# Kernel tuning notes

Hardware: AMD Instinct MI355X
Metric: run time of the kernel (lower is better)

The kernel has to match this reference:

```python
import math
import jax, jax.numpy as jnp
import numpy as np

B, T, C = 2, 2048, 2048
H, G = 16, 4          # n_head, n_group
HKV = H // G          # kv heads
HD = C // H           # head dim = 128

def setup_inputs() -> dict:
    key = jax.random.key(0)
    ks = jax.random.split(key, 4)
    s = 0.02  # realistic init scale
    return {
        "x": jax.random.normal(ks[0], (B, T, C), jnp.float32),
        "Wkv": jax.random.normal(ks[1], (C, 2 * C // G), jnp.float32) * s,
        "bkv": jnp.zeros((2 * C // G,), jnp.float32),
        "Wq": jax.random.normal(ks[2], (C, C), jnp.float32) * s,
        "bq": jnp.zeros((C,), jnp.float32),
        "Wp": jax.random.normal(ks[3], (C, C), jnp.float32) * s,
        "bp": jnp.zeros((C,), jnp.float32),
    }

def _expand_kv(t):
    # (B,T,HKV*HD) -> replicate each kv head G times -> (B,H,T,HD)
    t = t.reshape(B, T, HKV, HD)
    t = jnp.broadcast_to(t[:, :, None], (B, T, G, HKV, HD)).reshape(B, T, H, HD)
    return t.transpose(0, 2, 1, 3)

def reference(x, Wkv, bkv, Wq, bq, Wp, bp):
    kv = x @ Wkv + bkv                      # (B,T,2C/G)
    k, v = jnp.split(kv, 2, axis=-1)
    q = (x @ Wq + bq).reshape(B, T, H, HD).transpose(0, 2, 1, 3)  # (B,H,T,HD)
    k = _expand_kv(k)
    v = _expand_kv(v)
    att = jnp.einsum('bhqd,bhkd->bhqk', q, k) * (1.0 / math.sqrt(HD))
    mask = jnp.tril(jnp.ones((T, T), bool))
    att = jnp.where(mask, att, -jnp.inf)
    att = jax.nn.softmax(att, axis=-1)
    y = jnp.einsum('bhqk,bhkd->bhqd', att, v)
    y = y.transpose(0, 2, 1, 3).reshape(B, T, C)
    return y @ Wp + bp
```

## Files before the change

### kernel.cpp

```cpp
#include <hip/hip_runtime.h>

#define Bv 2
#define Tv 2048
#define Cv 2048
#define Hv 16
#define HKVv 4
#define HDv 128

typedef __attribute__((ext_vector_type(8))) __bf16 bf16x8;
typedef __attribute__((ext_vector_type(4))) float floatx4;

__device__ __forceinline__ unsigned short f2b(float f) {
  unsigned int x = __float_as_uint(f);
  x += 0x7fffu + ((x >> 16) & 1u);
  return (unsigned short)(x >> 16);
}

#define MFMA(a, b, c) __builtin_amdgcn_mfma_f32_16x16x32_bf16((a), (b), (c), 0, 0, 0)

__device__ __forceinline__ void gld_lds16(const void* g, void* l) {
  __builtin_amdgcn_global_load_lds((const __attribute__((address_space(1))) void*)g,
                                   (__attribute__((address_space(3))) void*)l, 16, 0, 0);
}

__global__ void cvt_kernel(const float* __restrict__ src, unsigned short* __restrict__ dst, int n4) {
  int i = blockIdx.x * blockDim.x + threadIdx.x;
  if (i < n4) {
    float4 f = ((const float4*)src)[i];
    ushort4 u;
    u.x = f2b(f.x); u.y = f2b(f.y); u.z = f2b(f.z); u.w = f2b(f.w);
    ((ushort4*)dst)[i] = u;
  }
}

__global__ void tcvt_kernel(const float* __restrict__ src, unsigned short* __restrict__ dst, int K, int N) {
  __shared__ float tile[32][33];
  int k0 = blockIdx.x * 32, n0 = blockIdx.y * 32;
  int tx = threadIdx.x, ty = threadIdx.y;
  for (int i = ty; i < 32; i += 8)
    tile[i][tx] = src[(size_t)(k0 + i) * N + n0 + tx];
  __syncthreads();
  for (int i = ty; i < 32; i += 8)
    dst[(size_t)(n0 + i) * K + k0 + tx] = f2b(tile[tx][i]);
}

__global__ __launch_bounds__(256) void gemm_qkv(
    const unsigned short* __restrict__ xb,
    const unsigned short* __restrict__ wq_t,
    const unsigned short* __restrict__ wkv_t,
    const float* __restrict__ bq, const float* __restrict__ bkv,
    unsigned short* __restrict__ qs,
    unsigned short* __restrict__ ks,
    unsigned short* __restrict__ vs) {
  __shared__ __align__(16) unsigned short Ash[128 * 32];
  __shared__ __align__(16) unsigned short Bsh[128 * 32];
  int tid = threadIdx.x;
  int wave = tid >> 6, lane = tid & 63;
  int c = lane & 15, quad = lane >> 4;
  int wr = (wave >> 1) * 64, wc = (wave & 1) * 64;
  int m0 = blockIdx.x * 128, n0 = blockIdx.y * 128;
  bool isq = (n0 < 2048);
  const unsigned short* wt = isq ? (wq_t + (size_t)n0 * 2048)
                                 : (wkv_t + (size_t)(n0 - 2048) * 2048);
  floatx4 zero4 = {0.f, 0.f, 0.f, 0.f};
  floatx4 acc[4][4];
#pragma unroll
  for (int i = 0; i < 4; i++)
#pragma unroll
    for (int j = 0; j < 4; j++) acc[i][j] = zero4;

  const unsigned short* Abase = xb + (size_t)m0 * 2048;
  int s0 = wave * 128 + lane, s1 = wave * 128 + 64 + lane;
  int r0 = s0 >> 2, kc0 = (s0 & 3) ^ (r0 & 3);
  int r1 = s1 >> 2, kc1 = (s1 & 3) ^ (r1 & 3);
  int swz3 = quad ^ (c & 3);

  for (int k0 = 0; k0 < 2048; k0 += 32) {
    gld_lds16(Abase + (size_t)r0 * 2048 + k0 + kc0 * 8, Ash + (size_t)(wave * 128) * 8);
    gld_lds16(Abase + (size_t)r1 * 2048 + k0 + kc1 * 8, Ash + (size_t)(wave * 128 + 64) * 8);
    gld_lds16(wt + (size_t)r0 * 2048 + k0 + kc0 * 8, Bsh + (size_t)(wave * 128) * 8);
    gld_lds16(wt + (size_t)r1 * 2048 + k0 + kc1 * 8, Bsh + (size_t)(wave * 128 + 64) * 8);
    __syncthreads();
    bf16x8 af[4], bfv[4];
#pragma unroll
    for (int i = 0; i < 4; i++)
      af[i] = *(const bf16x8*)(&Ash[(wr + i * 16 + c) * 32 + swz3 * 8]);
#pragma unroll
    for (int j = 0; j < 4; j++)
      bfv[j] = *(const bf16x8*)(&Bsh[(wc + j * 16 + c) * 32 + swz3 * 8]);
#pragma unroll
    for (int i = 0; i < 4; i++)
#pragma unroll
      for (int j = 0; j < 4; j++)
        acc[i][j] = MFMA(af[i], bfv[j], acc[i][j]);
    __syncthreads();
  }

#pragma unroll
  for (int i = 0; i < 4; i++) {
#pragma unroll
    for (int j = 0; j < 4; j++) {
#pragma unroll
      for (int r = 0; r < 4; r++) {
        int m = m0 + wr + i * 16 + quad * 4 + r;
        int n = n0 + wc + j * 16 + c;
        int bidx = m >> 11, t = m & 2047;
        float val = acc[i][j][r];
        if (isq) {
          val = (val + bq[n]) * 0.08838834764831845f;
          int hh = n >> 7, d = n & 127;
          qs[((size_t)((bidx * Hv + hh) * Tv) + t) * HDv + d] = f2b(val);
        } else {
          int n2 = n - 2048;
          val += bkv[n2];
          if (n2 < 512) {
            int hh = n2 >> 7, d = n2 & 127;
            ks[((size_t)((bidx * HKVv + hh) * Tv) + t) * HDv + d] = f2b(val);
          } else {
            int n3 = n2 - 512;
            int hh = n3 >> 7, d = n3 & 127;
            vs[((size_t)((bidx * HKVv + hh) * HDv) + d) * Tv + t] = f2b(val);
          }
        }
      }
    }
  }
}

__global__ __launch_bounds__(256, 4) void attn_kernel(
    const unsigned short* __restrict__ qs,
    const unsigned short* __restrict__ ks,
    const unsigned short* __restrict__ vs,
    unsigned short* __restrict__ ys) {
  __shared__ __align__(16) unsigned short Ksh[64 * 128];
  __shared__ __align__(16) unsigned short Vsh[128 * 64];
  __shared__ __align__(16) unsigned short Psh[4][16 * 64];

  int qt = blockIdx.x, h = blockIdx.y, b = blockIdx.z;
  int hkv = h & (HKVv - 1);
  int tid = threadIdx.x;
  int wave = tid >> 6, lane = tid & 63;
  int c = lane & 15, quad = lane >> 4;
  int q0w = qt * 64 + wave * 16;
  int qrow = q0w + c;
  int swz = c & 7;

  const unsigned short* qptr = qs + ((size_t)((b * Hv + h) * Tv) + q0w) * HDv;
  const unsigned short* kbase = ks + (size_t)((b * HKVv + hkv) * Tv) * HDv;
  const unsigned short* vbase = vs + (size_t)((b * HKVv + hkv) * HDv) * Tv;

  bf16x8 qf[4];
#pragma unroll
  for (int kc = 0; kc < 4; kc++)
    qf[kc] = *(const bf16x8*)(qptr + (size_t)c * HDv + kc * 32 + quad * 8);

  floatx4 zero4 = {0.f, 0.f, 0.f, 0.f};
  floatx4 o[8];
#pragma unroll
  for (int dt = 0; dt < 8; dt++) o[dt] = zero4;
  float M = -1e30f, L = 0.f;

  unsigned short* Pw = &Psh[wave][0];
  int ntiles = qt + 1;

  for (int kt = 0; kt < ntiles; kt++) {
    int kv0 = kt * 64;
#pragma unroll
    for (int i = 0; i < 4; i++) {
      int slot = wave * 256 + i * 64 + lane;
      int n = slot >> 4, g = (slot & 15) ^ (n & 7);
      gld_lds16(kbase + (size_t)(kv0 + n) * HDv + g * 8, Ksh + (size_t)(wave * 256 + i * 64) * 8);
    }
#pragma unroll
    for (int i = 0; i < 4; i++) {
      int slot = wave * 256 + i * 64 + lane;
      int n = slot >> 3, g = (slot & 7) ^ (n & 7);
      gld_lds16(vbase + (size_t)n * Tv + kv0 + g * 8, Vsh + (size_t)(wave * 256 + i * 64) * 8);
    }
    __syncthreads();

    bool active = (kv0 <= q0w + 15);
    if (active) {
      floatx4 st[4];
#pragma unroll
      for (int jj = 0; jj < 4; jj++) st[jj] = zero4;
#pragma unroll
      for (int kc = 0; kc < 4; kc++) {
#pragma unroll
        for (int jj = 0; jj < 4; jj++) {
          bf16x8 kf = *(const bf16x8*)(&Ksh[(jj * 16 + c) * 128 + (((kc * 4 + quad) ^ swz) * 8)]);
          st[jj] = MFMA(kf, qf[kc], st[jj]);
        }
      }
      if (kv0 + 63 > q0w) {
#pragma unroll
        for (int jj = 0; jj < 4; jj++) {
          int kvb = kv0 + jj * 16 + quad * 4;
#pragma unroll
          for (int r = 0; r < 4; r++)
            if (kvb + r > qrow) st[jj][r] = -1e30f;
        }
      }
      float mx = -1e30f;
#pragma unroll
      for (int jj = 0; jj < 4; jj++) {
        mx = fmaxf(mx, fmaxf(fmaxf(st[jj][0], st[jj][1]), fmaxf(st[jj][2], st[jj][3])));
      }
      mx = fmaxf(mx, __shfl_xor(mx, 16));
      mx = fmaxf(mx, __shfl_xor(mx, 32));
      float Mn = fmaxf(M, mx);
      float al = __expf(M - Mn);
      M = Mn;
      float l = 0.f;
#pragma unroll
      for (int jj = 0; jj < 4; jj++) {
        float p0 = __expf(st[jj][0] - Mn);
        float p1 = __expf(st[jj][1] - Mn);
        float p2 = __expf(st[jj][2] - Mn);
        float p3 = __expf(st[jj][3] - Mn);
        l += (p0 + p1) + (p2 + p3);
        unsigned int lo = (unsigned int)f2b(p0) | ((unsigned int)f2b(p1) << 16);
        unsigned int hi = (unsigned int)f2b(p2) | ((unsigned int)f2b(p3) << 16);
        int g = (jj * 2 + (quad >> 1)) ^ swz;
        *(uint2*)(&Pw[c * 64 + g * 8 + (quad & 1) * 4]) = make_uint2(lo, hi);
      }
      l += __shfl_xor(l, 16);
      l += __shfl_xor(l, 32);
      L = L * al + l;
#pragma unroll
      for (int dt = 0; dt < 8; dt++) o[dt] *= al;
#pragma unroll
      for (int kc2 = 0; kc2 < 2; kc2++) {
        bf16x8 pf = *(const bf16x8*)(&Pw[c * 64 + (((kc2 * 4 + quad) ^ swz) * 8)]);
#pragma unroll
        for (int dt = 0; dt < 8; dt++) {
          bf16x8 vf = *(const bf16x8*)(&Vsh[(dt * 16 + c) * 64 + (((kc2 * 4 + quad) ^ swz) * 8)]);
          o[dt] = MFMA(vf, pf, o[dt]);
        }
      }
    }
    __syncthreads();
  }

  float Li = 1.0f / L;
  size_t rowbase = ((size_t)(b * Tv + qrow)) * Cv + h * HDv;
#pragma unroll
  for (int dt = 0; dt < 8; dt++) {
    unsigned int lo = (unsigned int)f2b(o[dt][0] * Li) | ((unsigned int)f2b(o[dt][1] * Li) << 16);
    unsigned int hi = (unsigned int)f2b(o[dt][2] * Li) | ((unsigned int)f2b(o[dt][3] * Li) << 16);
    *(uint2*)(&ys[rowbase + dt * 16 + quad * 4]) = make_uint2(lo, hi);
  }
}

__global__ __launch_bounds__(256) void gemm_proj(
    const unsigned short* __restrict__ ys,
    const unsigned short* __restrict__ wp_t,
    const float* __restrict__ bp,
    float* __restrict__ out) {
  __shared__ __align__(16) unsigned short Ash[128 * 32];
  __shared__ __align__(16) unsigned short Bsh[128 * 32];
  int tid = threadIdx.x;
  int wave = tid >> 6, lane = tid & 63;
  int c = lane & 15, quad = lane >> 4;
  int wr = (wave >> 1) * 64, wc = (wave & 1) * 64;
  int m0 = blockIdx.x * 128, n0 = blockIdx.y * 128;
  floatx4 zero4 = {0.f, 0.f, 0.f, 0.f};
  floatx4 acc[4][4];
#pragma unroll
  for (int i = 0; i < 4; i++)
#pragma unroll
    for (int j = 0; j < 4; j++) acc[i][j] = zero4;

  const unsigned short* Abase = ys + (size_t)m0 * 2048;
  const unsigned short* Bbase = wp_t + (size_t)n0 * 2048;
  int s0 = wave * 128 + lane, s1 = wave * 128 + 64 + lane;
  int r0 = s0 >> 2, kc0 = (s0 & 3) ^ (r0 & 3);
  int r1 = s1 >> 2, kc1 = (s1 & 3) ^ (r1 & 3);
  int swz3 = quad ^ (c & 3);

  for (int k0 = 0; k0 < 2048; k0 += 32) {
    gld_lds16(Abase + (size_t)r0 * 2048 + k0 + kc0 * 8, Ash + (size_t)(wave * 128) * 8);
    gld_lds16(Abase + (size_t)r1 * 2048 + k0 + kc1 * 8, Ash + (size_t)(wave * 128 + 64) * 8);
    gld_lds16(Bbase + (size_t)r0 * 2048 + k0 + kc0 * 8, Bsh + (size_t)(wave * 128) * 8);
    gld_lds16(Bbase + (size_t)r1 * 2048 + k0 + kc1 * 8, Bsh + (size_t)(wave * 128 + 64) * 8);
    __syncthreads();
    bf16x8 af[4], bfv[4];
#pragma unroll
    for (int i = 0; i < 4; i++)
      af[i] = *(const bf16x8*)(&Ash[(wr + i * 16 + c) * 32 + swz3 * 8]);
#pragma unroll
    for (int j = 0; j < 4; j++)
      bfv[j] = *(const bf16x8*)(&Bsh[(wc + j * 16 + c) * 32 + swz3 * 8]);
#pragma unroll
    for (int i = 0; i < 4; i++)
#pragma unroll
      for (int j = 0; j < 4; j++)
        acc[i][j] = MFMA(af[i], bfv[j], acc[i][j]);
    __syncthreads();
  }

#pragma unroll
  for (int i = 0; i < 4; i++) {
#pragma unroll
    for (int j = 0; j < 4; j++) {
#pragma unroll
      for (int r = 0; r < 4; r++) {
        int m = m0 + wr + i * 16 + quad * 4 + r;
        int n = n0 + wc + j * 16 + c;
        out[(size_t)m * 2048 + n] = acc[i][j][r] + bp[n];
      }
    }
  }
}

extern "C" void kernel_launch(void* const* d_in, const int* in_sizes, int n_in,
                              void* d_out, int out_size, void* d_ws, size_t ws_size,
                              hipStream_t stream) {
  (void)in_sizes; (void)n_in; (void)out_size; (void)ws_size;
  const float* x   = (const float*)d_in[0];
  const float* Wkv = (const float*)d_in[1];
  const float* bkv = (const float*)d_in[2];
  const float* Wq  = (const float*)d_in[3];
  const float* bq  = (const float*)d_in[4];
  const float* Wp  = (const float*)d_in[5];
  const float* bp  = (const float*)d_in[6];
  float* out = (float*)d_out;

  char* ws = (char*)d_ws;
  unsigned short* xb    = (unsigned short*)(ws + 0);
  unsigned short* wq_t  = (unsigned short*)(ws + 16777216);
  unsigned short* wkv_t = (unsigned short*)(ws + 25165824);
  unsigned short* wp_t  = (unsigned short*)(ws + 29360128);
  unsigned short* qs    = (unsigned short*)(ws + 37748736);
  unsigned short* ks    = (unsigned short*)(ws + 54525952);
  unsigned short* vs    = (unsigned short*)(ws + 58720256);
  unsigned short* ysbuf = (unsigned short*)(ws + 62914560);

  cvt_kernel<<<8192, 256, 0, stream>>>(x, xb, 2097152);
  tcvt_kernel<<<dim3(64, 64), dim3(32, 8), 0, stream>>>(Wq, wq_t, 2048, 2048);
  tcvt_kernel<<<dim3(64, 32), dim3(32, 8), 0, stream>>>(Wkv, wkv_t, 2048, 1024);
  tcvt_kernel<<<dim3(64, 64), dim3(32, 8), 0, stream>>>(Wp, wp_t, 2048, 2048);
  gemm_qkv<<<dim3(32, 24), 256, 0, stream>>>(xb, wq_t, wkv_t, bq, bkv, qs, ks, vs);
  attn_kernel<<<dim3(32, 16, 2), 256, 0, stream>>>(qs, ks, vs, ysbuf);
  gemm_proj<<<dim3(32, 16), 256, 0, stream>>>(ysbuf, wp_t, bp, out);
}
```

Baseline: 401.7 us.

## Rework attention with 32x32 MFMA, 128-row query tiles, and double-buffered K/V

The attention kernel now uses 32x32x16 bf16 MFMA instructions with 32 query rows per wave and 128 per block, halving the grid. K/V tiles are double-buffered in LDS so the next tile's global-to-LDS loads overlap the current tile's compute. The P matrix is passed between lanes with cross-lane shuffles instead of an LDS round trip, and blocks are launched heaviest causal tile first. The cost is higher register and LDS use (launch bounds cut from 4 to 2 blocks per CU) and fewer blocks, which may reduce occupancy and load balance.

```diff
diff --git a/kernel.cpp b/kernel.cpp
--- a/kernel.cpp
+++ b/kernel.cpp
@@ -9,6 +9,7 @@
 
 typedef __attribute__((ext_vector_type(8))) __bf16 bf16x8;
 typedef __attribute__((ext_vector_type(4))) float floatx4;
+typedef __attribute__((ext_vector_type(16))) float floatx16;
 
 __device__ __forceinline__ unsigned short f2b(float f) {
   unsigned int x = __float_as_uint(f);
@@ -17,6 +18,7 @@
 }
 
 #define MFMA(a, b, c) __builtin_amdgcn_mfma_f32_16x16x32_bf16((a), (b), (c), 0, 0, 0)
+#define MFMA32(a, b, c) __builtin_amdgcn_mfma_f32_32x32x16_bf16((a), (b), (c), 0, 0, 0)
 
 __device__ __forceinline__ void gld_lds16(const void* g, void* l) {
   __builtin_amdgcn_global_load_lds((const __attribute__((address_space(1))) void*)g,
@@ -127,115 +129,144 @@
   }
 }
 
-__global__ __launch_bounds__(256, 4) void attn_kernel(
+__global__ __launch_bounds__(256, 2) void attn_kernel(
     const unsigned short* __restrict__ qs,
     const unsigned short* __restrict__ ks,
     const unsigned short* __restrict__ vs,
     unsigned short* __restrict__ ys) {
-  __shared__ __align__(16) unsigned short Ksh[64 * 128];
-  __shared__ __align__(16) unsigned short Vsh[128 * 64];
-  __shared__ __align__(16) unsigned short Psh[4][16 * 64];
-
-  int qt = blockIdx.x, h = blockIdx.y, b = blockIdx.z;
+  __shared__ __align__(16) unsigned short Ksh[2][64 * 128];
+  __shared__ __align__(16) unsigned short Vsh[2][128 * 64];
+
+  int qt = (gridDim.x - 1) - blockIdx.x;
+  int h = blockIdx.y, b = blockIdx.z;
   int hkv = h & (HKVv - 1);
   int tid = threadIdx.x;
   int wave = tid >> 6, lane = tid & 63;
-  int c = lane & 15, quad = lane >> 4;
-  int q0w = qt * 64 + wave * 16;
-  int qrow = q0w + c;
-  int swz = c & 7;
+  int q5 = lane & 31, hi = lane >> 5;
+  int q0w = qt * 128 + wave * 32;
+  int qrow = q0w + q5;
 
   const unsigned short* qptr = qs + ((size_t)((b * Hv + h) * Tv) + q0w) * HDv;
   const unsigned short* kbase = ks + (size_t)((b * HKVv + hkv) * Tv) * HDv;
   const unsigned short* vbase = vs + (size_t)((b * HKVv + hkv) * HDv) * Tv;
 
-  bf16x8 qf[4];
-#pragma unroll
-  for (int kc = 0; kc < 4; kc++)
-    qf[kc] = *(const bf16x8*)(qptr + (size_t)c * HDv + kc * 32 + quad * 8);
-
-  floatx4 zero4 = {0.f, 0.f, 0.f, 0.f};
-  floatx4 o[8];
-#pragma unroll
-  for (int dt = 0; dt < 8; dt++) o[dt] = zero4;
+  bf16x8 qf[8];
+#pragma unroll
+  for (int kc = 0; kc < 8; kc++)
+    qf[kc] = *(const bf16x8*)(qptr + (size_t)q5 * HDv + kc * 16 + hi * 8);
+
+  floatx16 o[4];
+#pragma unroll
+  for (int dt = 0; dt < 4; dt++)
+#pragma unroll
+    for (int r = 0; r < 16; r++) o[dt][r] = 0.f;
   float M = -1e30f, L = 0.f;
 
-  unsigned short* Pw = &Psh[wave][0];
-  int ntiles = qt + 1;
+  int kOff[4], vOff[4];
+#pragma unroll
+  for (int i = 0; i < 4; i++) {
+    int s = wave * 256 + i * 64 + lane;
+    int rk = s >> 4, gk = (s & 15) ^ (rk & 15);
+    kOff[i] = rk * 128 + gk * 8;
+    int rv = s >> 3, gv = (s & 7) ^ (rv & 7);
+    vOff[i] = rv * Tv + gv * 8;
+  }
+  int ldsBase = (wave * 256) * 8;
+
+  int ntiles = 2 * qt + 2;
+
+#pragma unroll
+  for (int i = 0; i < 4; i++) gld_lds16(kbase + kOff[i], &Ksh[0][0] + ldsBase + i * 512);
+#pragma unroll
+  for (int i = 0; i < 4; i++) gld_lds16(vbase + vOff[i], &Vsh[0][0] + ldsBase + i * 512);
+  __syncthreads();
 
   for (int kt = 0; kt < ntiles; kt++) {
     int kv0 = kt * 64;
-#pragma unroll
-    for (int i = 0; i < 4; i++) {
-      int slot = wave * 256 + i * 64 + lane;
-      int n = slot >> 4, g = (slot & 15) ^ (n & 7);
-      gld_lds16(kbase + (size_t)(kv0 + n) * HDv + g * 8, Ksh + (size_t)(wave * 256 + i * 64) * 8);
-    }
-#pragma unroll
-    for (int i = 0; i < 4; i++) {
-      int slot = wave * 256 + i * 64 + lane;
-      int n = slot >> 3, g = (slot & 7) ^ (n & 7);
-      gld_lds16(vbase + (size_t)n * Tv + kv0 + g * 8, Vsh + (size_t)(wave * 256 + i * 64) * 8);
-    }
-    __syncthreads();
-
-    bool active = (kv0 <= q0w + 15);
-    if (active) {
-      floatx4 st[4];
-#pragma unroll
-      for (int jj = 0; jj < 4; jj++) st[jj] = zero4;
-#pragma unroll
-      for (int kc = 0; kc < 4; kc++) {
-#pragma unroll
-        for (int jj = 0; jj < 4; jj++) {
-          bf16x8 kf = *(const bf16x8*)(&Ksh[(jj * 16 + c) * 128 + (((kc * 4 + quad) ^ swz) * 8)]);
-          st[jj] = MFMA(kf, qf[kc], st[jj]);
+    int cur = kt & 1;
+    if (kt + 1 < ntiles) {
+      int kv1 = (kt + 1) * 64;
+#pragma unroll
+      for (int i = 0; i < 4; i++)
+        gld_lds16(kbase + (size_t)kv1 * 128 + kOff[i], &Ksh[cur ^ 1][0] + ldsBase + i * 512);
+#pragma unroll
+      for (int i = 0; i < 4; i++)
+        gld_lds16(vbase + kv1 + vOff[i], &Vsh[cur ^ 1][0] + ldsBase + i * 512);
+    }
+
+    if (kv0 <= q0w + 31) {
+      const unsigned short* Kb = &Ksh[cur][0];
+      const unsigned short* Vb = &Vsh[cur][0];
+      floatx16 st[2];
+#pragma unroll
+      for (int sub = 0; sub < 2; sub++) {
+#pragma unroll
+        for (int r = 0; r < 16; r++) st[sub][r] = 0.f;
+#pragma unroll
+        for (int kc = 0; kc < 8; kc++) {
+          bf16x8 kf = *(const bf16x8*)(&Kb[(sub * 32 + q5) * 128 + (((kc * 2 + hi) ^ (q5 & 15)) * 8)]);
+          st[sub] = MFMA32(kf, qf[kc], st[sub]);
         }
       }
       if (kv0 + 63 > q0w) {
-#pragma unroll
-        for (int jj = 0; jj < 4; jj++) {
-          int kvb = kv0 + jj * 16 + quad * 4;
-#pragma unroll
-          for (int r = 0; r < 4; r++)
-            if (kvb + r > qrow) st[jj][r] = -1e30f;
+        int kvb = kv0 + 4 * hi - qrow;
+#pragma unroll
+        for (int sub = 0; sub < 2; sub++) {
+#pragma unroll
+          for (int r = 0; r < 16; r++) {
+            int roff = (r & 3) + 8 * (r >> 2) + sub * 32;
+            if (kvb + roff > 0) st[sub][r] = -1e30f;
+          }
         }
       }
       float mx = -1e30f;
 #pragma unroll
-      for (int jj = 0; jj < 4; jj++) {
-        mx = fmaxf(mx, fmaxf(fmaxf(st[jj][0], st[jj][1]), fmaxf(st[jj][2], st[jj][3])));
-      }
-      mx = fmaxf(mx, __shfl_xor(mx, 16));
+      for (int sub = 0; sub < 2; sub++)
+#pragma unroll
+        for (int r = 0; r < 16; r++) mx = fmaxf(mx, st[sub][r]);
       mx = fmaxf(mx, __shfl_xor(mx, 32));
       float Mn = fmaxf(M, mx);
       float al = __expf(M - Mn);
       M = Mn;
+      float p[2][16];
       float l = 0.f;
 #pragma unroll
-      for (int jj = 0; jj < 4; jj++) {
-        float p0 = __expf(st[jj][0] - Mn);
-        float p1 = __expf(st[jj][1] - Mn);
-        float p2 = __expf(st[jj][2] - Mn);
-        float p3 = __expf(st[jj][3] - Mn);
-        l += (p0 + p1) + (p2 + p3);
-        unsigned int lo = (unsigned int)f2b(p0) | ((unsigned int)f2b(p1) << 16);
-        unsigned int hi = (unsigned int)f2b(p2) | ((unsigned int)f2b(p3) << 16);
-        int g = (jj * 2 + (quad >> 1)) ^ swz;
-        *(uint2*)(&Pw[c * 64 + g * 8 + (quad & 1) * 4]) = make_uint2(lo, hi);
-      }
-      l += __shfl_xor(l, 16);
+      for (int sub = 0; sub < 2; sub++)
+#pragma unroll
+        for (int r = 0; r < 16; r++) {
+          p[sub][r] = __expf(st[sub][r] - Mn);
+          l += p[sub][r];
+        }
       l += __shfl_xor(l, 32);
       L = L * al + l;
 #pragma unroll
-      for (int dt = 0; dt < 8; dt++) o[dt] *= al;
-#pragma unroll
-      for (int kc2 = 0; kc2 < 2; kc2++) {
-        bf16x8 pf = *(const bf16x8*)(&Pw[c * 64 + (((kc2 * 4 + quad) ^ swz) * 8)]);
-#pragma unroll
-        for (int dt = 0; dt < 8; dt++) {
-          bf16x8 vf = *(const bf16x8*)(&Vsh[(dt * 16 + c) * 64 + (((kc2 * 4 + quad) ^ swz) * 8)]);
-          o[dt] = MFMA(vf, pf, o[dt]);
+      for (int dt = 0; dt < 4; dt++)
+#pragma unroll
+        for (int r = 0; r < 16; r++) o[dt][r] *= al;
+      unsigned int pk[8][2];
+#pragma unroll
+      for (int sub = 0; sub < 2; sub++)
+#pragma unroll
+        for (int m = 0; m < 4; m++) {
+          pk[sub * 4 + m][0] = (unsigned int)f2b(p[sub][m * 4 + 0]) | ((unsigned int)f2b(p[sub][m * 4 + 1]) << 16);
+          pk[sub * 4 + m][1] = (unsigned int)f2b(p[sub][m * 4 + 2]) | ((unsigned int)f2b(p[sub][m * 4 + 3]) << 16);
+        }
+#pragma unroll
+      for (int ksp = 0; ksp < 4; ksp++) {
+        int ml = 2 * ksp + hi;
+        int mr = 2 * ksp + (hi ^ 1);
+        unsigned int r0 = __shfl_xor((int)pk[mr][0], 32);
+        unsigned int r1 = __shfl_xor((int)pk[mr][1], 32);
+        unsigned int w0 = hi ? r0 : pk[ml][0];
+        unsigned int w1 = hi ? r1 : pk[ml][1];
+        unsigned int w2 = hi ? pk[ml][0] : r0;
+        unsigned int w3 = hi ? pk[ml][1] : r1;
+        union { unsigned int u[4]; bf16x8 v; } pf;
+        pf.u[0] = w0; pf.u[1] = w1; pf.u[2] = w2; pf.u[3] = w3;
+#pragma unroll
+        for (int dt = 0; dt < 4; dt++) {
+          bf16x8 vf = *(const bf16x8*)(&Vb[(dt * 32 + q5) * 64 + (((ksp * 2 + hi) ^ (q5 & 7)) * 8)]);
+          o[dt] = MFMA32(vf, pf.v, o[dt]);
         }
       }
     }
@@ -245,10 +276,14 @@
   float Li = 1.0f / L;
   size_t rowbase = ((size_t)(b * Tv + qrow)) * Cv + h * HDv;
 #pragma unroll
-  for (int dt = 0; dt < 8; dt++) {
-    unsigned int lo = (unsigned int)f2b(o[dt][0] * Li) | ((unsigned int)f2b(o[dt][1] * Li) << 16);
-    unsigned int hi = (unsigned int)f2b(o[dt][2] * Li) | ((unsigned int)f2b(o[dt][3] * Li) << 16);
-    *(uint2*)(&ys[rowbase + dt * 16 + quad * 4]) = make_uint2(lo, hi);
+  for (int dt = 0; dt < 4; dt++) {
+#pragma unroll
+    for (int m = 0; m < 4; m++) {
+      int d = dt * 32 + 8 * m + 4 * hi;
+      unsigned int lo = (unsigned int)f2b(o[dt][m * 4 + 0] * Li) | ((unsigned int)f2b(o[dt][m * 4 + 1] * Li) << 16);
+      unsigned int hi2 = (unsigned int)f2b(o[dt][m * 4 + 2] * Li) | ((unsigned int)f2b(o[dt][m * 4 + 3] * Li) << 16);
+      *(uint2*)(&ys[rowbase + d]) = make_uint2(lo, hi2);
+    }
   }
 }
 
@@ -341,6 +376,6 @@
   tcvt_kernel<<<dim3(64, 32), dim3(32, 8), 0, stream>>>(Wkv, wkv_t, 2048, 1024);
   tcvt_kernel<<<dim3(64, 64), dim3(32, 8), 0, stream>>>(Wp, wp_t, 2048, 2048);
   gemm_qkv<<<dim3(32, 24), 256, 0, stream>>>(xb, wq_t, wkv_t, bq, bkv, qs, ks, vs);
-  attn_kernel<<<dim3(32, 16, 2), 256, 0, stream>>>(qs, ks, vs, ysbuf);
+  attn_kernel<<<dim3(16, 16, 2), 256, 0, stream>>>(qs, ks, vs, ysbuf);
   gemm_proj<<<dim3(32, 16), 256, 0, stream>>>(ysbuf, wp_t, bp, out);
 }
```

Measured after the change: 455.5 us. +13.4%, slower.

## Double-buffer K/V tiles with 32-wide blocks and balance causal work across heads

Applied to the files above, without the earlier changes.

The attention kernel now prefetches the next K/V tile into a second LDS buffer while computing on the current one, with the KV tile width halved from 64 to 32 to keep LDS use in check. Query tile order is reversed for heads with bit 3 set, so long and short causal rows mix across the grid. The intent is to hide global-to-LDS load latency and reduce the load-imbalance tail. The cost is twice as many loop iterations, each with less MFMA work to amortize barriers and softmax overhead.

```diff
diff --git a/kernel.cpp b/kernel.cpp
--- a/kernel.cpp
+++ b/kernel.cpp
@@ -132,18 +132,19 @@
     const unsigned short* __restrict__ ks,
     const unsigned short* __restrict__ vs,
     unsigned short* __restrict__ ys) {
-  __shared__ __align__(16) unsigned short Ksh[64 * 128];
-  __shared__ __align__(16) unsigned short Vsh[128 * 64];
-  __shared__ __align__(16) unsigned short Psh[4][16 * 64];
-
-  int qt = blockIdx.x, h = blockIdx.y, b = blockIdx.z;
+  __shared__ __align__(16) unsigned short Ksh[2][32 * 128];
+  __shared__ __align__(16) unsigned short Vsh[2][128 * 32];
+  __shared__ __align__(16) unsigned short Psh[4][16 * 32];
+
+  int x = blockIdx.x, h = blockIdx.y, b = blockIdx.z;
+  int qt = (h & 8) ? (31 - x) : x;
   int hkv = h & (HKVv - 1);
   int tid = threadIdx.x;
   int wave = tid >> 6, lane = tid & 63;
   int c = lane & 15, quad = lane >> 4;
   int q0w = qt * 64 + wave * 16;
   int qrow = q0w + c;
-  int swz = c & 7;
+  int swzK = c & 7, swzV = c & 3;
 
   const unsigned short* qptr = qs + ((size_t)((b * Hv + h) * Tv) + q0w) * HDv;
   const unsigned short* kbase = ks + (size_t)((b * HKVv + hkv) * Tv) * HDv;
@@ -161,51 +162,64 @@
   float M = -1e30f, L = 0.f;
 
   unsigned short* Pw = &Psh[wave][0];
-  int ntiles = qt + 1;
+
+  int kOff[2], vOff[2];
+#pragma unroll
+  for (int i = 0; i < 2; i++) {
+    int s = wave * 128 + i * 64 + lane;
+    int rk = s >> 4, gk = (s & 15) ^ (rk & 7);
+    kOff[i] = rk * 128 + gk * 8;
+    int rv = s >> 2, gv = (s & 3) ^ (rv & 3);
+    vOff[i] = rv * Tv + gv * 8;
+  }
+  int ldsBase = (wave * 128) * 8;
+
+  int ntiles = 2 * qt + 2;
+
+#pragma unroll
+  for (int i = 0; i < 2; i++) gld_lds16(kbase + kOff[i], &Ksh[0][0] + ldsBase + i * 512);
+#pragma unroll
+  for (int i = 0; i < 2; i++) gld_lds16(vbase + vOff[i], &Vsh[0][0] + ldsBase + i * 512);
+  __syncthreads();
 
   for (int kt = 0; kt < ntiles; kt++) {
-    int kv0 = kt * 64;
-#pragma unroll
-    for (int i = 0; i < 4; i++) {
-      int slot = wave * 256 + i * 64 + lane;
-      int n = slot >> 4, g = (slot & 15) ^ (n & 7);
-      gld_lds16(kbase + (size_t)(kv0 + n) * HDv + g * 8, Ksh + (size_t)(wave * 256 + i * 64) * 8);
+    int kv0 = kt * 32;
+    int cur = kt & 1;
+    if (kt + 1 < ntiles) {
+      int kv1 = (kt + 1) * 32;
+#pragma unroll
+      for (int i = 0; i < 2; i++)
+        gld_lds16(kbase + (size_t)kv1 * 128 + kOff[i], &Ksh[cur ^ 1][0] + ldsBase + i * 512);
+#pragma unroll
+      for (int i = 0; i < 2; i++)
+        gld_lds16(vbase + kv1 + vOff[i], &Vsh[cur ^ 1][0] + ldsBase + i * 512);
     }
-#pragma unroll
-    for (int i = 0; i < 4; i++) {
-      int slot = wave * 256 + i * 64 + lane;
-      int n = slot >> 3, g = (slot & 7) ^ (n & 7);
-      gld_lds16(vbase + (size_t)n * Tv + kv0 + g * 8, Vsh + (size_t)(wave * 256 + i * 64) * 8);
-    }
-    __syncthreads();
-
-    bool active = (kv0 <= q0w + 15);
-    if (active) {
-      floatx4 st[4];
-#pragma unroll
-      for (int jj = 0; jj < 4; jj++) st[jj] = zero4;
+
+    if (kv0 <= q0w + 15) {
+      const unsigned short* Kb = &Ksh[cur][0];
+      const unsigned short* Vb = &Vsh[cur][0];
+      floatx4 st[2] = {zero4, zero4};
 #pragma unroll
       for (int kc = 0; kc < 4; kc++) {
 #pragma unroll
-        for (int jj = 0; jj < 4; jj++) {
-          bf16x8 kf = *(const bf16x8*)(&Ksh[(jj * 16 + c) * 128 + (((kc * 4 + quad) ^ swz) * 8)]);
-          st[jj] = MFMA(kf, qf[kc], st[jj]);
+        for (int sub = 0; sub < 2; sub++) {
+          bf16x8 kf = *(const bf16x8*)(&Kb[(sub * 16 + c) * 128 + (((kc * 4 + quad) ^ swzK) * 8)]);
+          st[sub] = MFMA(kf, qf[kc], st[sub]);
         }
       }
-      if (kv0 + 63 > q0w) {
-#pragma unroll
-        for (int jj = 0; jj < 4; jj++) {
-          int kvb = kv0 + jj * 16 + quad * 4;
+      if (kv0 + 31 > q0w) {
+#pragma unroll
+        for (int sub = 0; sub < 2; sub++) {
+          int kvb = kv0 + sub * 16 + quad * 4;
 #pragma unroll
           for (int r = 0; r < 4; r++)
-            if (kvb + r > qrow) st[jj][r] = -1e30f;
+            if (kvb + r > qrow) st[sub][r] = -1e30f;
         }
       }
       float mx = -1e30f;
 #pragma unroll
-      for (int jj = 0; jj < 4; jj++) {
-        mx = fmaxf(mx, fmaxf(fmaxf(st[jj][0], st[jj][1]), fmaxf(st[jj][2], st[jj][3])));
-      }
+      for (int sub = 0; sub < 2; sub++)
+        mx = fmaxf(mx, fmaxf(fmaxf(st[sub][0], st[sub][1]), fmaxf(st[sub][2], st[sub][3])));
       mx = fmaxf(mx, __shfl_xor(mx, 16));
       mx = fmaxf(mx, __shfl_xor(mx, 32));
       float Mn = fmaxf(M, mx);
@@ -213,30 +227,27 @@
       M = Mn;
       float l = 0.f;
 #pragma unroll
-      for (int jj = 0; jj < 4; jj++) {
-        float p0 = __expf(st[jj][0] - Mn);
-        float p1 = __expf(st[jj][1] - Mn);
-        float p2 = __expf(st[jj][2] - Mn);
-        float p3 = __expf(st[jj][3] - Mn);
+      for (int sub = 0; sub < 2; sub++) {
+        float p0 = __expf(st[sub][0] - Mn);
+        float p1 = __expf(st[sub][1] - Mn);
+        float p2 = __expf(st[sub][2] - Mn);
+        float p3 = __expf(st[sub][3] - Mn);
         l += (p0 + p1) + (p2 + p3);
         unsigned int lo = (unsigned int)f2b(p0) | ((unsigned int)f2b(p1) << 16);
         unsigned int hi = (unsigned int)f2b(p2) | ((unsigned int)f2b(p3) << 16);
-        int g = (jj * 2 + (quad >> 1)) ^ swz;
-        *(uint2*)(&Pw[c * 64 + g * 8 + (quad & 1) * 4]) = make_uint2(lo, hi);
+        int g = (sub * 2 + (quad >> 1)) ^ swzV;
+        *(uint2*)(&Pw[c * 32 + g * 8 + (quad & 1) * 4]) = make_uint2(lo, hi);
       }
       l += __shfl_xor(l, 16);
       l += __shfl_xor(l, 32);
       L = L * al + l;
 #pragma unroll
       for (int dt = 0; dt < 8; dt++) o[dt] *= al;
-#pragma unroll
-      for (int kc2 = 0; kc2 < 2; kc2++) {
-        bf16x8 pf = *(const bf16x8*)(&Pw[c * 64 + (((kc2 * 4 + quad) ^ swz) * 8)]);
-#pragma unroll
-        for (int dt = 0; dt < 8; dt++) {
-          bf16x8 vf = *(const bf16x8*)(&Vsh[(dt * 16 + c) * 64 + (((kc2 * 4 + quad) ^ swz) * 8)]);
-          o[dt] = MFMA(vf, pf, o[dt]);
-        }
+      bf16x8 pf = *(const bf16x8*)(&Pw[c * 32 + ((quad ^ swzV) * 8)]);
+#pragma unroll
+      for (int dt = 0; dt < 8; dt++) {
+        bf16x8 vf = *(const bf16x8*)(&Vb[(dt * 16 + c) * 32 + ((quad ^ swzV) * 8)]);
+        o[dt] = MFMA(vf, pf, o[dt]);
       }
     }
     __syncthreads();
@@ -247,8 +258,8 @@
 #pragma unroll
   for (int dt = 0; dt < 8; dt++) {
     unsigned int lo = (unsigned int)f2b(o[dt][0] * Li) | ((unsigned int)f2b(o[dt][1] * Li) << 16);
-    unsigned int hi = (unsigned int)f2b(o[dt][2] * Li) | ((unsigned int)f2b(o[dt][3] * Li) << 16);
-    *(uint2*)(&ys[rowbase + dt * 16 + quad * 4]) = make_uint2(lo, hi);
+    unsigned int hi2 = (unsigned int)f2b(o[dt][2] * Li) | ((unsigned int)f2b(o[dt][3] * Li) << 16);
+    *(uint2*)(&ys[rowbase + dt * 16 + quad * 4]) = make_uint2(lo, hi2);
   }
 }
 
```

Result: faster. 369.7 us (-8.0%).
